# Kernel tuning notes

Measured on AMD Instinct MI355X. Metric: run time of the kernel, lower is better.

## Reference

```python
import jax, jax.numpy as jnp
import numpy as np
from jax import lax

# norse LIFParameters defaults: dt=1e-3, tau_mem_inv=100, tau_syn_inv=200, v_leak=0, v_reset=0
ALPHA = 100.0
DT_TM = 0.1   # dt * tau_mem_inv
DT_TS = 0.2   # dt * tau_syn_inv

@jax.custom_vjp
def superspike(x):
    # Heaviside forward, SuperSpike surrogate gradient backward
    return (x > 0).astype(x.dtype)

def _ss_fwd(x):
    return superspike(x), x

def _ss_bwd(x, g):
    return (g / (ALPHA * jnp.abs(x) + 1.0) ** 2,)

superspike.defvjp(_ss_fwd, _ss_bwd)

def lif_step(inp, v, i, v_th):
    # norse lif_feed_forward_step (feedforward LIF cell)
    v_dec = v + DT_TM * (i - v)           # v_leak = 0
    i_dec = i * (1.0 - DT_TS)
    z = superspike(v_dec - v_th)
    v_new = (1.0 - z) * v_dec             # reset to v_reset = 0 on spike
    return z, v_new, i_dec + inp

def conv2d(x, w):
    return lax.conv_general_dilated(x, w, (1, 1), 'VALID',
                                    dimension_numbers=('NCHW', 'OIHW', 'NCHW'))

def avg_pool2(x):
    s = lax.reduce_window(x, jnp.zeros((), x.dtype), lax.add,
                          (1, 1, 2, 2), (1, 1, 2, 2), 'VALID')
    return s * jnp.asarray(0.25, x.dtype)

def setup_inputs() -> dict:
    key = jax.random.key(0)
    ks = jax.random.split(key, 6)
    x = jax.random.uniform(ks[0], (40, 256, 1, 28, 28), dtype=jnp.float32)
    # kaiming-ish scales (1/sqrt(fan_in))
    w_conv1 = jax.random.normal(ks[1], (20, 1, 3, 3), jnp.float32) * (1.0 / np.sqrt(9))
    w_conv2 = jax.random.normal(ks[2], (50, 20, 3, 3), jnp.float32) * (1.0 / np.sqrt(180))
    w_fc1 = jax.random.normal(ks[3], (500, 6050), jnp.float32) * (1.0 / np.sqrt(6050))
    w_fc2 = jax.random.normal(ks[4], (200, 500), jnp.float32) * (1.0 / np.sqrt(500))
    w_fc_out = jax.random.normal(ks[5], (10, 200), jnp.float32) * (1.0 / np.sqrt(200))
    return {"x": x, "w_conv1": w_conv1, "w_conv2": w_conv2,
            "w_fc1": w_fc1, "w_fc2": w_fc2, "w_fc_out": w_fc_out}

def reference(x, w_conv1, w_conv2, w_fc1, w_fc2, w_fc_out):
    T, B = x.shape[0], x.shape[1]
    dt = x.dtype
    z0 = jnp.zeros((B, 20, 26, 26), dt)
    z1 = jnp.zeros((B, 50, 11, 11), dt)
    z2 = jnp.zeros((B, 500), dt)
    z3 = jnp.zeros((B, 200), dt)
    zo = jnp.zeros((B, 10), dt)
    carry0 = (z0, z0, z1, z1, z2, z2, z3, z3, zo, zo)

    def step(carry, xt):
        v0, i0, v1, i1, v2, i2, v3, i3, vo, io = carry
        z = conv2d(xt, w_conv1)
        z, v0, i0 = lif_step(z, v0, i0, 0.2)
        z = avg_pool2(z)
        z = conv2d(z, w_conv2)
        z, v1, i1 = lif_step(z, v1, i1, 0.2)
        z = z.reshape(B, -1)                      # [B, 50*11*11]
        z = z @ w_fc1.T
        z, v2, i2 = lif_step(z, v2, i2, 0.1)
        z = z @ w_fc2.T
        z, v3, i3 = lif_step(z, v3, i3, 0.05)
        z = z @ w_fc_out.T
        # LICell (norse li_feed_forward_step): output is decayed membrane voltage
        v_dec = vo + DT_TM * (io - vo)
        i_new = io * (1.0 - DT_TS) + z
        return (v0, i0, v1, i1, v2, i2, v3, i3, v_dec, i_new), v_dec

    _, voltages = lax.scan(step, carry0, x)
    return voltages  # [T, B, output_neurons]
```

## Files before the change

### kernel.cpp

```cpp
#include <hip/hip_runtime.h>
#include <hip/hip_bf16.h>

typedef _Float16 f16x8 __attribute__((ext_vector_type(8)));
typedef float f32x4  __attribute__((ext_vector_type(4)));
typedef int   i32x4  __attribute__((ext_vector_type(4)));
typedef unsigned short u16x4 __attribute__((ext_vector_type(4)));

#define T_STEPS 40
#define BATCH   256
#define S2LO    0.000244140625f
#define WQ_INV  (2080768.0f/0.103f)
#define WQ_S    (0.103f/2080768.0f)

__device__ __forceinline__ unsigned short f2h_bits(float f) {
    union { _Float16 h; unsigned short u; } c; c.h = (_Float16)f; return c.u;
}

__device__ __forceinline__ float lif_update(float inp, float& v, float& i, float vth) {
    float vd = __fadd_rn(v, __fmul_rn(0.1f, __fsub_rn(i, v)));
    float id = __fmul_rn(0.8f, i);
    float z  = (vd > vth) ? 1.0f : 0.0f;
    v = (vd > vth) ? 0.0f : vd;
    i = __fadd_rn(id, inp);
    return z;
}

__device__ __forceinline__ void llds16(const void* g, void* l) {
    __builtin_amdgcn_global_load_lds(
        (const __attribute__((address_space(1))) unsigned int*)g,
        (__attribute__((address_space(3))) unsigned int*)l, 16, 0, 0);
}

__global__ __launch_bounds__(512) void k_conv1(
    const float* __restrict__ x,
    const float* __restrict__ w1,
    unsigned char* __restrict__ s0,
    const float* __restrict__ wf1,
    const float* __restrict__ wf2,
    signed char* __restrict__ W1,
    unsigned short* __restrict__ W2)
{
    if (blockIdx.y >= 256) {
        int pid = (blockIdx.y - 256)*8 + blockIdx.x;
        for (int idx = pid*512 + threadIdx.x; idx < 3342336; idx += 106496) {
            if (idx < 3211264) {
                int n = idx / 6272, k = idx - n*6272;
                int oc = k / 124, pos = k - oc*124;
                float v = (n < 500 && oc < 50 && pos < 121)
                          ? wf1[n*6050 + oc*121 + pos] : 0.f;
                float a = v * WQ_INV;
                int q2 = __float2int_rn(a * (1.0f/16384.0f));
                q2 = q2 < -127 ? -127 : (q2 > 127 ? 127 : q2);
                float r1 = a - (float)q2 * 16384.0f;
                int q1 = __float2int_rn(r1 * (1.0f/128.0f));
                q1 = q1 < -127 ? -127 : (q1 > 127 ? 127 : q1);
                float r0 = r1 - (float)q1 * 128.0f;
                int q0 = __float2int_rn(r0);
                q0 = q0 < -127 ? -127 : (q0 > 127 ? 127 : q0);
                W1[idx]             = (signed char)q0;
                W1[idx + 3211264]   = (signed char)q1;
                W1[idx + 2*3211264] = (signed char)q2;
            } else {
                int i2 = idx - 3211264;
                int n = i2 >> 9, k = i2 & 511;
                float v = (n < 200 && k < 500) ? wf2[n*500 + k] : 0.f;
                _Float16 h = (_Float16)v;
                float r1 = (v - (float)h) * 4096.0f;
                union { _Float16 h; unsigned short u; } ch, cl;
                ch.h = h; cl.h = (_Float16)r1;
                W2[i2] = ch.u;
                W2[i2 + 131072] = cl.u;
            }
        }
        return;
    }

    const int b    = blockIdx.y;
    const int tid  = threadIdx.x;
    const int cell = blockIdx.x*512 + tid;
    const int pos  = cell / 24;
    const int oc   = cell - pos*24;
    const bool active = (pos < 169) && (oc < 20);
    const int pr   = pos / 13, q = pos - pr*13;
    const int r0   = 2*pr, c0 = 2*q;

    __shared__ __align__(16) float xl[4][784];
    const bool stager = tid < 196;

    float wr[9];
    if (active) {
        #pragma unroll
        for (int j = 0; j < 9; ++j) wr[j] = w1[oc*9 + j];
    }
    float vs[2][2], is[2][2];
    #pragma unroll
    for (int dr = 0; dr < 2; ++dr)
        #pragma unroll
        for (int dc = 0; dc < 2; ++dc) { vs[dr][dc] = 0.f; is[dr][dc] = 0.f; }

    float4 pA, pB;
    if (stager) {
        *(float4*)&xl[0][tid*4] = ((const float4*)(x + (size_t)(0*BATCH + b)*784))[tid];
        *(float4*)&xl[1][tid*4] = ((const float4*)(x + (size_t)(1*BATCH + b)*784))[tid];
        pA = ((const float4*)(x + (size_t)(2*BATCH + b)*784))[tid];
        pB = ((const float4*)(x + (size_t)(3*BATCH + b)*784))[tid];
    }

    for (int t = 0; t < T_STEPS; ++t) {
        __syncthreads();
        if (stager) {
            if (t + 2 < T_STEPS) *(float4*)&xl[(t+2)&3][tid*4] = pA;
            pA = pB;
            if (t + 4 < T_STEPS)
                pB = ((const float4*)(x + (size_t)((t+4)*BATCH + b)*784))[tid];
        }
        const float* xc = xl[t&3];
        size_t base = (size_t)(t*BATCH + b) * 4096;

        unsigned char outb = 0;
        if (active) {
            float tle[4][4];
            #pragma unroll
            for (int r = 0; r < 4; ++r) {
                float2 t01 = *(const float2*)&xc[(r0 + r)*28 + c0];
                float2 t23 = *(const float2*)&xc[(r0 + r)*28 + c0 + 2];
                tle[r][0] = t01.x; tle[r][1] = t01.y;
                tle[r][2] = t23.x; tle[r][3] = t23.y;
            }
            int zsum = 0;
            #pragma unroll
            for (int dr = 0; dr < 2; ++dr)
                #pragma unroll
                for (int dc = 0; dc < 2; ++dc) {
                    float acc = 0.f;
                    #pragma unroll
                    for (int kr = 0; kr < 3; ++kr)
                        #pragma unroll
                        for (int kc = 0; kc < 3; ++kc)
                            acc += tle[dr+kr][dc+kc] * wr[kr*3+kc];
                    float z = lif_update(acc, vs[dr][dc], is[dr][dc], 0.2f);
                    zsum += (z > 0.5f) ? 1 : 0;
                }
            outb = (unsigned char)zsum;
        }
        s0[base + cell] = outb;
    }
}

__global__ __launch_bounds__(256, 4) void k_conv2(
    const unsigned char* __restrict__ s0,
    const float* __restrict__ w2,
    unsigned char* __restrict__ z1)
{
    const int b    = blockIdx.x >> 2;
    const int quad = blockIdx.x & 3;
    const int tid  = threadIdx.x;
    const int wv   = tid >> 6;
    const int lane = tid & 63;
    const int l15  = lane & 15;
    const int kg   = lane >> 4;
    const int wm   = wv;

    __shared__ __align__(16) unsigned short w2h[16*232];
    __shared__ __align__(16) unsigned short w2m[16*232];
    __shared__ __align__(16) unsigned short sIn[2*4096];

    for (int s = tid; s < 16*232; s += 256) {
        int ocw = s / 232, kk = s % 232;
        int g = kk / 24, ic = kk % 24;
        int oc = quad*16 + ocw;
        float val = 0.f;
        if (oc < 50 && g < 9 && ic < 20) val = 0.25f * w2[(oc*20 + ic)*9 + g];
        _Float16 h = (_Float16)val;
        float r1 = (val - (float)h) * 4096.0f;
        union { _Float16 h; unsigned short u; } ch, cm;
        ch.h = h; cm.h = (_Float16)r1;
        w2h[s] = ch.u;
        w2m[s] = cm.u;
    }

    f16x8 bfrH[7];
    int addrA[2][7];
    #pragma unroll
    for (int mt = 0; mt < 2; ++mt) {
        int pos = wm*32 + mt*16 + l15;
        #pragma unroll
        for (int kt = 0; kt < 7; ++kt) {
            int k = kt*32 + kg*8;
            int g = k / 24, o = k - g*24;
            if (pos <= 120 && g <= 8) {
                int in_idx = pos + 2*(pos/11) + 13*(g/3) + (g % 3);
                addrA[mt][kt] = in_idx*48 + o*2;
            } else addrA[mt][kt] = 8128;
        }
    }

    {
        const unsigned char* srow = s0 + (size_t)(0*BATCH + b)*4096;
        uint4 raw = *(const uint4*)(srow + tid*16);
        unsigned short hv[16];
        #pragma unroll
        for (int w = 0; w < 4; ++w) {
            unsigned int u = ((const unsigned int*)&raw)[w];
            #pragma unroll
            for (int j = 0; j < 4; ++j)
                hv[w*4+j] = f2h_bits((float)((u >> (8*j)) & 0xFFu));
        }
        unsigned short* dst = sIn + tid*16;
        *(f16x8*)dst       = *(const f16x8*)&hv[0];
        *(f16x8*)(dst + 8) = *(const f16x8*)&hv[8];
    }
    __syncthreads();

    #pragma unroll
    for (int kt = 0; kt < 7; ++kt)
        bfrH[kt] = *(const f16x8*)&w2h[l15*232 + kt*32 + kg*8];

    float vst[2][4], ist[2][4];
    #pragma unroll
    for (int mt = 0; mt < 2; ++mt)
        #pragma unroll
        for (int r = 0; r < 4; ++r) { vst[mt][r] = 0.f; ist[mt][r] = 0.f; }

    const f32x4 zero4 = {0.f, 0.f, 0.f, 0.f};

    for (int t = 0; t < T_STEPS; ++t) {
        if (t > 0) __syncthreads();

        uint4 raw;
        if (t + 1 < T_STEPS)
            raw = *(const uint4*)(s0 + (size_t)((t+1)*BATCH + b)*4096 + tid*16);

        const char* curB = (const char*)(sIn + (t&1)*4096);

        f32x4 acch[2], accl[2];
        #pragma unroll
        for (int mt = 0; mt < 2; ++mt) { acch[mt] = zero4; accl[mt] = zero4; }

        #pragma unroll
        for (int kt = 0; kt < 7; ++kt) {
            f16x8 bm = *(const f16x8*)&w2m[l15*232 + kt*32 + kg*8];
            #pragma unroll
            for (int mt = 0; mt < 2; ++mt) {
                f16x8 a = *(const f16x8*)(curB + addrA[mt][kt]);
                acch[mt] = __builtin_amdgcn_mfma_f32_16x16x32_f16(
                    a, bfrH[kt], acch[mt], 0, 0, 0);
                accl[mt] = __builtin_amdgcn_mfma_f32_16x16x32_f16(
                    a, bm, accl[mt], 0, 0, 0);
            }
        }

        size_t rowoff = (size_t)(t*BATCH + b) * 6272;
        #pragma unroll
        for (int mt = 0; mt < 2; ++mt) {
            int posb = wm*32 + mt*16 + kg*4;
            int ocn = quad*16 + l15;
            unsigned char pk[4];
            #pragma unroll
            for (int r = 0; r < 4; ++r) {
                float inp = __fadd_rn(acch[mt][r], __fmul_rn(S2LO, accl[mt][r]));
                float z = lif_update(inp, vst[mt][r], ist[mt][r], 0.2f);
                int pos = posb + r;
                pk[r] = (pos <= 120 && z > 0.5f) ? (unsigned char)1 : (unsigned char)0;
            }
            if (ocn < 50 && posb < 121)
                *(uchar4*)(z1 + rowoff + ocn*124 + posb) = *(const uchar4*)&pk[0];
        }
        if (quad == 0 && tid < 72) z1[rowoff + 6200 + tid] = 0;

        if (t + 1 < T_STEPS) {
            unsigned short hv[16];
            #pragma unroll
            for (int w = 0; w < 4; ++w) {
                unsigned int u = ((const unsigned int*)&raw)[w];
                #pragma unroll
                for (int j = 0; j < 4; ++j)
                    hv[w*4+j] = f2h_bits((float)((u >> (8*j)) & 0xFFu));
            }
            unsigned short* dst = sIn + ((t+1)&1)*4096 + tid*16;
            *(f16x8*)dst       = *(const f16x8*)&hv[0];
            *(f16x8*)(dst + 8) = *(const f16x8*)&hv[8];
        }
    }
}

__global__ __launch_bounds__(256, 4) void k_gemm_fc1(
    const unsigned char* __restrict__ A,
    const signed char* __restrict__ Bq,
    float* __restrict__ P,
    int mb0)
{
    __shared__ __align__(16) unsigned char As[64*128];
    __shared__ __align__(16) unsigned char Bs[3*64*128];

    const int tid  = threadIdx.x;
    const int lane = tid & 63;
    const int wv   = tid >> 6;
    const int wm   = wv & 1, wn = wv >> 1;
    const int l15  = lane & 15, kg = lane >> 4;
    const int mbase = (blockIdx.x + mb0) * 64;
    const int nbase = blockIdx.y * 64;
    const int kz    = blockIdx.z;
    const int kb0   = kz * 3200;
    const int kiters = 25 - kz;

    float* Pz = P + (size_t)kz * 5242880;

    i32x4 acc[3][2][2];
    #pragma unroll
    for (int p = 0; p < 3; ++p)
        #pragma unroll
        for (int mt = 0; mt < 2; ++mt)
            #pragma unroll
            for (int nt = 0; nt < 2; ++nt) acc[p][mt][nt] = (i32x4){0,0,0,0};

    const int rowS = tid >> 3;
    const int chk  = tid & 7;
    char* ldsA = (char*)As + (size_t)wv*1024;
    char* ldsB = (char*)Bs + (size_t)wv*1024;

    for (int ki = 0; ki < kiters; ++ki) {
        int kb = kb0 + ki * 128;
        #pragma unroll
        for (int c = 0; c < 2; ++c) {
            int rl = c*32 + rowS;
            llds16(A + (size_t)(mbase + rl)*6272 + kb + 16*(chk ^ (rl & 7)),
                   ldsA + c*4096);
        }
        #pragma unroll
        for (int p = 0; p < 3; ++p)
            #pragma unroll
            for (int c2 = 0; c2 < 2; ++c2) {
                int rl = c2*32 + rowS;
                llds16(Bq + (size_t)p*3211264 + (size_t)(nbase + rl)*6272
                          + kb + 16*(chk ^ (rl & 7)),
                       ldsB + (p*2 + c2)*4096);
            }
        __syncthreads();

        #pragma unroll
        for (int ks = 0; ks < 2; ++ks) {
            i32x4 afv[2], bfv[3][2];
            #pragma unroll
            for (int nt = 0; nt < 2; ++nt) {
                int rb = wn*32 + nt*16 + l15;
                int off = rb*128 + 16*((ks*4 + kg) ^ (rb & 7));
                #pragma unroll
                for (int p = 0; p < 3; ++p)
                    bfv[p][nt] = *(const i32x4*)&Bs[p*8192 + off];
            }
            #pragma unroll
            for (int mt = 0; mt < 2; ++mt) {
                int ra = wm*32 + mt*16 + l15;
                afv[mt] = *(const i32x4*)&As[ra*128 + 16*((ks*4 + kg) ^ (ra & 7))];
            }
            #pragma unroll
            for (int p = 0; p < 3; ++p)
                #pragma unroll
                for (int mt = 0; mt < 2; ++mt)
                    #pragma unroll
                    for (int nt = 0; nt < 2; ++nt)
                        acc[p][mt][nt] = __builtin_amdgcn_mfma_i32_16x16x64_i8(
                            afv[mt], bfv[p][nt], acc[p][mt][nt], 0, 0, 0);
        }
        __syncthreads();
    }

    #pragma unroll
    for (int mt = 0; mt < 2; ++mt) {
        int m0 = mbase + wm*32 + mt*16 + kg*4;
        #pragma unroll
        for (int nt = 0; nt < 2; ++nt) {
            int n = nbase + wn*32 + nt*16 + l15;
            #pragma unroll
            for (int r = 0; r < 4; ++r) {
                float d = __fadd_rn(
                    __fadd_rn(__fmul_rn(16384.0f, (float)acc[2][mt][nt][r]),
                              __fmul_rn(128.0f,   (float)acc[1][mt][nt][r])),
                    (float)acc[0][mt][nt][r]);
                Pz[(size_t)(m0 + r)*512 + n] = __fmul_rn(WQ_S, d);
            }
        }
    }
}

__global__ __launch_bounds__(256, 6) void k_gemm_fc2(
    const unsigned short* __restrict__ A,
    const unsigned short* __restrict__ B,
    float* __restrict__ C)
{
    __shared__ __align__(16) unsigned short As[64*64];
    __shared__ __align__(16) unsigned short Bh[64*64];
    __shared__ __align__(16) unsigned short Bl[64*64];

    const int tid  = threadIdx.x;
    const int lane = tid & 63;
    const int wv   = tid >> 6;
    const int wm   = wv & 1, wn = wv >> 1;
    const int l15  = lane & 15, kg = lane >> 4;
    const int mbase = blockIdx.x * 64;
    const int nbase = blockIdx.y * 64;
    const unsigned short* Blo = B + 131072;

    const f32x4 zero4 = {0.f, 0.f, 0.f, 0.f};
    f32x4 acch[2][2], accl[2][2];
    #pragma unroll
    for (int mt = 0; mt < 2; ++mt)
        #pragma unroll
        for (int nt = 0; nt < 2; ++nt) { acch[mt][nt] = zero4; accl[mt][nt] = zero4; }

    const int rowS = tid >> 3;
    const int chk  = tid & 7;
    char* ldsA = (char*)As + (size_t)wv*1024;
    char* ldsH = (char*)Bh + (size_t)wv*1024;
    char* ldsL = (char*)Bl + (size_t)wv*1024;

    for (int ki = 0; ki < 8; ++ki) {
        int kb = ki * 64;
        #pragma unroll
        for (int c = 0; c < 2; ++c) {
            int rl = c*32 + rowS;
            int sw = (chk ^ (rl & 7)) * 8;
            llds16(A   + (size_t)(mbase + rl)*512 + kb + sw, ldsA + c*4096);
            llds16(B   + (size_t)(nbase + rl)*512 + kb + sw, ldsH + c*4096);
            llds16(Blo + (size_t)(nbase + rl)*512 + kb + sw, ldsL + c*4096);
        }
        __syncthreads();
        #pragma unroll
        for (int kt = 0; kt < 2; ++kt) {
            f16x8 bh[2], bl[2], afv[2];
            #pragma unroll
            for (int nt = 0; nt < 2; ++nt) {
                int rb = wn*32 + nt*16 + l15;
                int ch = ((kt*4 + kg) ^ (rb & 7)) * 8;
                bh[nt] = *(const f16x8*)&Bh[rb*64 + ch];
                bl[nt] = *(const f16x8*)&Bl[rb*64 + ch];
            }
            #pragma unroll
            for (int mt = 0; mt < 2; ++mt) {
                int ra = wm*32 + mt*16 + l15;
                int ch = ((kt*4 + kg) ^ (ra & 7)) * 8;
                afv[mt] = *(const f16x8*)&As[ra*64 + ch];
            }
            #pragma unroll
            for (int mt = 0; mt < 2; ++mt)
                #pragma unroll
                for (int nt = 0; nt < 2; ++nt) {
                    acch[mt][nt] = __builtin_amdgcn_mfma_f32_16x16x32_f16(
                        afv[mt], bh[nt], acch[mt][nt], 0, 0, 0);
                    accl[mt][nt] = __builtin_amdgcn_mfma_f32_16x16x32_f16(
                        afv[mt], bl[nt], accl[mt][nt], 0, 0, 0);
                }
        }
        __syncthreads();
    }

    #pragma unroll
    for (int mt = 0; mt < 2; ++mt) {
        int m0 = mbase + wm*32 + mt*16 + kg*4;
        #pragma unroll
        for (int nt = 0; nt < 2; ++nt) {
            int n = nbase + wn*32 + nt*16 + l15;
            #pragma unroll
            for (int r = 0; r < 4; ++r) {
                float s = __fadd_rn(acch[mt][nt][r], __fmul_rn(S2LO, accl[mt][nt][r]));
                C[(size_t)(m0 + r)*256 + n] = s;
            }
        }
    }
}

__global__ void k_lif_scan(
    const float* __restrict__ c0, size_t pstride,
    unsigned short* __restrict__ zout,
    int ld, int nvalid, float vth, float pscale)
{
    int b = blockIdx.y;
    int n = blockIdx.x*blockDim.x + threadIdx.x;
    float v = 0.f, cur = 0.f;
    const float* sx = c0 + (size_t)b*ld + n;
    const float* sy = sx + pstride;
    const size_t step = (size_t)BATCH*ld;
    float x0 = sx[0],      y0 = sy[0];
    float x1 = sx[step],   y1 = sy[step];
    float x2 = sx[2*step], y2 = sy[2*step];
    float x3 = sx[3*step], y3 = sy[3*step];

    #define LIF_SUB(J, XV, YV)                                                \
        {                                                                     \
            float s = __fadd_rn(XV, __fmul_rn(pscale, YV));                   \
            float z = lif_update(s, v, cur, vth);                             \
            zout[(size_t)((t+J)*BATCH + b)*ld + n] =                          \
                (n < nvalid && z > 0.5f) ? (unsigned short)0x3C00             \
                                         : (unsigned short)0;                 \
            if (t + J + 4 < T_STEPS) {                                        \
                XV = sx[(size_t)(t + J + 4)*step];                            \
                YV = sy[(size_t)(t + J + 4)*step];                            \
            }                                                                 \
        }

    for (int t = 0; t < T_STEPS; t += 4) {
        LIF_SUB(0, x0, y0);
        LIF_SUB(1, x1, y1);
        LIF_SUB(2, x2, y2);
        LIF_SUB(3, x3, y3);
    }
    #undef LIF_SUB
}

__global__ __launch_bounds__(256) void k_sc2_fcout_li(
    const float* __restrict__ c3,
    const float* __restrict__ wfo,
    float* __restrict__ out)
{
    const int b   = blockIdx.x;
    const int tid = threadIdx.x;
    __shared__ __align__(16) float wfoL[2000];
    __shared__ unsigned char z3L[T_STEPS*200];
    __shared__ float sL[400];

    for (int i = tid; i < 2000; i += 256) wfoL[i] = wfo[i];

    if (tid < 200) {
        const float* sx = c3 + (size_t)b*256 + tid;
        const size_t step = (size_t)BATCH*256;
        float v = 0.f, cur = 0.f;
        float x0 = sx[0], x1 = sx[step], x2 = sx[2*step], x3 = sx[3*step];

        #define SC2_SUB(J, XV)                                                \
            {                                                                 \
                float z = lif_update(XV, v, cur, 0.05f);                      \
                z3L[(t+J)*200 + tid] = (z > 0.5f) ? 1 : 0;                    \
                if (t + J + 4 < T_STEPS)                                      \
                    XV = sx[(size_t)(t + J + 4)*step];                        \
            }

        for (int t = 0; t < T_STEPS; t += 4) {
            SC2_SUB(0, x0);
            SC2_SUB(1, x1);
            SC2_SUB(2, x2);
            SC2_SUB(3, x3);
        }
        #undef SC2_SUB
    }
    __syncthreads();

    #pragma unroll
    for (int rep = 0; rep < 2; ++rep) {
        int task = tid + rep*256;
        if (task < 400) {
            int t = task / 10, n = task - t*10;
            float acc = 0.f;
            for (int k = 0; k < 200; k += 4) {
                uchar4 zb = *(const uchar4*)&z3L[t*200 + k];
                float4 wv = *(const float4*)&wfoL[n*200 + k];
                acc = __fadd_rn(acc, zb.x ? wv.x : 0.f);
                acc = __fadd_rn(acc, zb.y ? wv.y : 0.f);
                acc = __fadd_rn(acc, zb.z ? wv.z : 0.f);
                acc = __fadd_rn(acc, zb.w ? wv.w : 0.f);
            }
            sL[t*10 + n] = acc;
        }
    }
    __syncthreads();

    if (tid < 10) {
        float vo = 0.f, io = 0.f;
        for (int t = 0; t < T_STEPS; ++t) {
            float vd = __fadd_rn(vo, __fmul_rn(0.1f, __fsub_rn(io, vo)));
            out[((size_t)(t*BATCH + b))*10 + tid] = vd;
            io = __fadd_rn(__fmul_rn(0.8f, io), sL[t*10 + tid]);
            vo = vd;
        }
    }
}

extern "C" void kernel_launch(void* const* d_in, const int* in_sizes, int n_in,
                              void* d_out, int out_size, void* d_ws, size_t ws_size,
                              hipStream_t stream) {
    (void)in_sizes; (void)n_in; (void)out_size; (void)ws_size;
    const float* x   = (const float*)d_in[0];
    const float* w1  = (const float*)d_in[1];
    const float* w2  = (const float*)d_in[2];
    const float* wf1 = (const float*)d_in[3];
    const float* wf2 = (const float*)d_in[4];
    const float* wfo = (const float*)d_in[5];
    char* ws = (char*)d_ws;

    unsigned char*  z1    = (unsigned char*)(ws);
    unsigned char*  s0    = (unsigned char*)(ws + 64225280);
    float*          c2p   = (float*)(ws + 74383360);
    signed char*    W1q   = (signed char*)(ws + 116326400);
    unsigned short* W2hi  = (unsigned short*)(ws + 125960192);
    unsigned short* z2    = (unsigned short*)(ws);
    float*          c3    = (float*)(ws + 10485760);

    k_conv1<<<dim3(8, 282), 512, 0, stream>>>(x, w1, s0, wf1, wf2, W1q, W2hi);
    k_conv2<<<1024, 256, 0, stream>>>(s0, w2, z1);

    k_gemm_fc1<<<dim3(80, 8, 2), 256, 0, stream>>>(z1, W1q, c2p, 0);
    k_gemm_fc1<<<dim3(80, 8, 2), 256, 0, stream>>>(z1, W1q, c2p, 80);
    k_lif_scan<<<dim3(2, 256), 256, 0, stream>>>(c2p, (size_t)5242880, z2, 512, 500, 0.1f, 1.0f);
    k_gemm_fc2<<<dim3(160, 4), 256, 0, stream>>>(z2, W2hi, c3);
    k_sc2_fcout_li<<<256, 256, 0, stream>>>(c3, wfo, (float*)d_out);
}
```

Measured before the change: 390.9 us.

## Split weight packing into own kernel, stage only needed input rows in conv1

Weight quantisation and packing for fc1 and fc2 moves out of the conv1 launch into a separate kernel that runs after conv2, and the packed weights now reuse the s0 workspace region. Each conv1 block now stages only the input rows its output positions need, which shrinks shared memory and global loads per block. The two fc1 GEMM launches are merged into a single grid. The aim is less shared memory and input traffic in conv1, a smaller workspace footprint and fewer launches, at the cost of an extra kernel launch for packing.

After: 366.0 us. 1.07x faster.

```diff
diff --git a/kernel.cpp b/kernel.cpp
--- a/kernel.cpp
+++ b/kernel.cpp
@@ -34,47 +34,8 @@
 __global__ __launch_bounds__(512) void k_conv1(
     const float* __restrict__ x,
     const float* __restrict__ w1,
-    unsigned char* __restrict__ s0,
-    const float* __restrict__ wf1,
-    const float* __restrict__ wf2,
-    signed char* __restrict__ W1,
-    unsigned short* __restrict__ W2)
+    unsigned char* __restrict__ s0)
 {
-    if (blockIdx.y >= 256) {
-        int pid = (blockIdx.y - 256)*8 + blockIdx.x;
-        for (int idx = pid*512 + threadIdx.x; idx < 3342336; idx += 106496) {
-            if (idx < 3211264) {
-                int n = idx / 6272, k = idx - n*6272;
-                int oc = k / 124, pos = k - oc*124;
-                float v = (n < 500 && oc < 50 && pos < 121)
-                          ? wf1[n*6050 + oc*121 + pos] : 0.f;
-                float a = v * WQ_INV;
-                int q2 = __float2int_rn(a * (1.0f/16384.0f));
-                q2 = q2 < -127 ? -127 : (q2 > 127 ? 127 : q2);
-                float r1 = a - (float)q2 * 16384.0f;
-                int q1 = __float2int_rn(r1 * (1.0f/128.0f));
-                q1 = q1 < -127 ? -127 : (q1 > 127 ? 127 : q1);
-                float r0 = r1 - (float)q1 * 128.0f;
-                int q0 = __float2int_rn(r0);
-                q0 = q0 < -127 ? -127 : (q0 > 127 ? 127 : q0);
-                W1[idx]             = (signed char)q0;
-                W1[idx + 3211264]   = (signed char)q1;
-                W1[idx + 2*3211264] = (signed char)q2;
-            } else {
-                int i2 = idx - 3211264;
-                int n = i2 >> 9, k = i2 & 511;
-                float v = (n < 200 && k < 500) ? wf2[n*500 + k] : 0.f;
-                _Float16 h = (_Float16)v;
-                float r1 = (v - (float)h) * 4096.0f;
-                union { _Float16 h; unsigned short u; } ch, cl;
-                ch.h = h; cl.h = (_Float16)r1;
-                W2[i2] = ch.u;
-                W2[i2 + 131072] = cl.u;
-            }
-        }
-        return;
-    }
-
     const int b    = blockIdx.y;
     const int tid  = threadIdx.x;
     const int cell = blockIdx.x*512 + tid;
@@ -82,10 +43,17 @@
     const int oc   = cell - pos*24;
     const bool active = (pos < 169) && (oc < 20);
     const int pr   = pos / 13, q = pos - pr*13;
-    const int r0   = 2*pr, c0 = 2*q;
-
-    __shared__ __align__(16) float xl[4][784];
-    const bool stager = tid < 196;
+    const int c0   = 2*q;
+
+    const int p0    = (blockIdx.x*512) / 24;
+    const int pmaxv = min((blockIdx.x*512 + 511) / 24, 168);
+    const int rlo   = 2*(p0/13);
+    const int rhi   = min(2*(pmaxv/13) + 3, 27);
+    const int nf4   = (rhi - rlo + 1) * 7;
+    const int rloc  = 2*pr - rlo;
+
+    __shared__ __align__(16) float xl[4][224];
+    const bool stager = tid < nf4;
 
     float wr[9];
     if (active) {
@@ -100,10 +68,11 @@
 
     float4 pA, pB;
     if (stager) {
-        *(float4*)&xl[0][tid*4] = ((const float4*)(x + (size_t)(0*BATCH + b)*784))[tid];
-        *(float4*)&xl[1][tid*4] = ((const float4*)(x + (size_t)(1*BATCH + b)*784))[tid];
-        pA = ((const float4*)(x + (size_t)(2*BATCH + b)*784))[tid];
-        pB = ((const float4*)(x + (size_t)(3*BATCH + b)*784))[tid];
+        const float* xr = x + (size_t)b*784 + rlo*28;
+        *(float4*)&xl[0][tid*4] = ((const float4*)(xr + 0*BATCH*784))[tid];
+        *(float4*)&xl[1][tid*4] = ((const float4*)(xr + 1ull*BATCH*784))[tid];
+        pA = ((const float4*)(xr + 2ull*BATCH*784))[tid];
+        pB = ((const float4*)(xr + 3ull*BATCH*784))[tid];
     }
 
     for (int t = 0; t < T_STEPS; ++t) {
@@ -112,7 +81,7 @@
             if (t + 2 < T_STEPS) *(float4*)&xl[(t+2)&3][tid*4] = pA;
             pA = pB;
             if (t + 4 < T_STEPS)
-                pB = ((const float4*)(x + (size_t)((t+4)*BATCH + b)*784))[tid];
+                pB = ((const float4*)(x + (size_t)((t+4)*BATCH + b)*784 + rlo*28))[tid];
         }
         const float* xc = xl[t&3];
         size_t base = (size_t)(t*BATCH + b) * 4096;
@@ -122,8 +91,8 @@
             float tle[4][4];
             #pragma unroll
             for (int r = 0; r < 4; ++r) {
-                float2 t01 = *(const float2*)&xc[(r0 + r)*28 + c0];
-                float2 t23 = *(const float2*)&xc[(r0 + r)*28 + c0 + 2];
+                float2 t01 = *(const float2*)&xc[(rloc + r)*28 + c0];
+                float2 t23 = *(const float2*)&xc[(rloc + r)*28 + c0 + 2];
                 tle[r][0] = t01.x; tle[r][1] = t01.y;
                 tle[r][2] = t23.x; tle[r][3] = t23.y;
             }
@@ -287,8 +256,7 @@
 __global__ __launch_bounds__(256, 4) void k_gemm_fc1(
     const unsigned char* __restrict__ A,
     const signed char* __restrict__ Bq,
-    float* __restrict__ P,
-    int mb0)
+    float* __restrict__ P)
 {
     __shared__ __align__(16) unsigned char As[64*128];
     __shared__ __align__(16) unsigned char Bs[3*64*128];
@@ -298,7 +266,7 @@
     const int wv   = tid >> 6;
     const int wm   = wv & 1, wn = wv >> 1;
     const int l15  = lane & 15, kg = lane >> 4;
-    const int mbase = (blockIdx.x + mb0) * 64;
+    const int mbase = blockIdx.x * 64;
     const int nbase = blockIdx.y * 64;
     const int kz    = blockIdx.z;
     const int kb0   = kz * 3200;
@@ -467,6 +435,42 @@
                 C[(size_t)(m0 + r)*256 + n] = s;
             }
         }
+    }
+}
+
+__global__ void k_pack_all(
+    const float* __restrict__ wf1, const float* __restrict__ wf2,
+    signed char* __restrict__ W1, unsigned short* __restrict__ W2)
+{
+    int idx = blockIdx.x*256 + threadIdx.x;
+    if (idx < 3211264) {
+        int n = idx / 6272, k = idx - n*6272;
+        int oc = k / 124, pos = k - oc*124;
+        float v = (n < 500 && oc < 50 && pos < 121) ? wf1[n*6050 + oc*121 + pos] : 0.f;
+        float a = v * WQ_INV;
+        int q2 = __float2int_rn(a * (1.0f/16384.0f));
+        q2 = q2 < -127 ? -127 : (q2 > 127 ? 127 : q2);
+        float r1 = a - (float)q2 * 16384.0f;
+        int q1 = __float2int_rn(r1 * (1.0f/128.0f));
+        q1 = q1 < -127 ? -127 : (q1 > 127 ? 127 : q1);
+        float r0 = r1 - (float)q1 * 128.0f;
+        int q0 = __float2int_rn(r0);
+        q0 = q0 < -127 ? -127 : (q0 > 127 ? 127 : q0);
+        W1[idx]             = (signed char)q0;
+        W1[idx + 3211264]   = (signed char)q1;
+        W1[idx + 2*3211264] = (signed char)q2;
+        return;
+    }
+    if (idx < 3211264 + 131072) {
+        int i2 = idx - 3211264;
+        int n = i2 >> 9, k = i2 & 511;
+        float v = (n < 200 && k < 500) ? wf2[n*500 + k] : 0.f;
+        _Float16 h = (_Float16)v;
+        float r1 = (v - (float)h) * 4096.0f;
+        union { _Float16 h; unsigned short u; } ch, cl;
+        ch.h = h; cl.h = (_Float16)r1;
+        W2[i2] = ch.u;
+        W2[i2 + 131072] = cl.u;
     }
 }
 
@@ -589,17 +593,18 @@
 
     unsigned char*  z1    = (unsigned char*)(ws);
     unsigned char*  s0    = (unsigned char*)(ws + 64225280);
+    signed char*    W1q   = (signed char*)(ws + 64225280);
+    unsigned short* W2hi  = (unsigned short*)(ws + 73859072);
     float*          c2p   = (float*)(ws + 74383360);
-    signed char*    W1q   = (signed char*)(ws + 116326400);
-    unsigned short* W2hi  = (unsigned short*)(ws + 125960192);
     unsigned short* z2    = (unsigned short*)(ws);
     float*          c3    = (float*)(ws + 10485760);
 
-    k_conv1<<<dim3(8, 282), 512, 0, stream>>>(x, w1, s0, wf1, wf2, W1q, W2hi);
+    k_conv1<<<dim3(8, 256), 512, 0, stream>>>(x, w1, s0);
     k_conv2<<<1024, 256, 0, stream>>>(s0, w2, z1);
 
-    k_gemm_fc1<<<dim3(80, 8, 2), 256, 0, stream>>>(z1, W1q, c2p, 0);
-    k_gemm_fc1<<<dim3(80, 8, 2), 256, 0, stream>>>(z1, W1q, c2p, 80);
+    k_pack_all<<<13056, 256, 0, stream>>>(wf1, wf2, W1q, W2hi);
+
+    k_gemm_fc1<<<dim3(160, 8, 2), 256, 0, stream>>>(z1, W1q, c2p);
     k_lif_scan<<<dim3(2, 256), 256, 0, stream>>>(c2p, (size_t)5242880, z2, 512, 500, 0.1f, 1.0f);
     k_gemm_fc2<<<dim3(160, 4), 256, 0, stream>>>(z2, W2hi, c3);
     k_sc2_fcout_li<<<256, 256, 0, stream>>>(c3, wfo, (float*)d_out);
```
